# Kernel tuning notes

Measured on AMD Instinct MI355X. Metric: run time of the kernel, lower is better.

The kernel has to match this reference:

```python
import jax, jax.numpy as jnp
import numpy as np
import math

N_ENTITIES = 200000
N_ITEMS = 100000
N_REL = 40
DIM = 64
N_HEADS = 2
DK = DIM // N_HEADS
N_EDGES = 1500000
K_EDGES = 256
K_ITEMS = 100


def setup_inputs() -> dict:
    key = jax.random.key(0)
    k1, k2, k3, k4, k5, k6 = jax.random.split(key, 6)
    entity_emb = jax.random.normal(k1, (N_ENTITIES, DIM), jnp.float32) * 0.1
    W_Q = jax.random.normal(k2, (DIM, DIM), jnp.float32) * (1.0 / math.sqrt(DIM))
    relation_emb = jax.random.normal(k3, (N_REL - 1, DIM), jnp.float32) * 0.1
    edge_index = jax.random.randint(k4, (2, N_EDGES), 0, N_ENTITIES, jnp.int32)
    # edge_type in [1, N_REL-1]: code indexes relation_emb[edge_type - 1]
    edge_type = jax.random.randint(k5, (N_EDGES,), 1, N_REL, jnp.int32)
    # uniform(0,1) driving the gumbel noise -log(-log(u)); clipped away from 0
    noise_u = jax.random.uniform(k6, (N_EDGES,), jnp.float32, 1e-9, 1.0)
    return {"entity_emb": entity_emb, "W_Q": W_Q, "relation_emb": relation_emb,
            "noise_u": noise_u, "edge_index": edge_index, "edge_type": edge_type}


def reference(entity_emb, W_Q, relation_emb, noise_u, edge_index, edge_type):
    head, tail = edge_index[0], edge_index[1]
    E = edge_index.shape[1]

    # --- norm_attn_computer (AttnHGCN): per-edge multi-head attention ---
    # project once on nodes, then gather (same math as (emb[head] @ W_Q))
    proj = entity_emb @ W_Q                               # [N, D]
    q = proj[head].reshape(E, N_HEADS, DK)                # [E, H, Dk]
    k = proj[tail].reshape(E, N_HEADS, DK)                # [E, H, Dk]
    rel = relation_emb[edge_type - 1].reshape(E, N_HEADS, DK)
    attn = jnp.sum(q * k * rel, axis=-1) / math.sqrt(DK)  # [E, H]
    edge_attn_logits = attn.mean(axis=-1)                 # [E]

    # scatter_softmax over head nodes, then multiply by head degree (norm)
    seg_max = jax.lax.stop_gradient(
        jax.ops.segment_max(edge_attn_logits, head, num_segments=N_ENTITIES))
    ex = jnp.exp(edge_attn_logits - seg_max[head])
    denom = jax.ops.segment_sum(ex, head, num_segments=N_ENTITIES)
    edge_attn_score = ex / denom[head]
    deg = jax.ops.segment_sum(jnp.ones_like(edge_attn_logits), head,
                              num_segments=N_ENTITIES)
    edge_attn_score = edge_attn_score * deg[head]         # [E]

    # --- attn logit sums per item (head + tail scatter_sum), topk 100 ---
    sum_by_node = (jax.ops.segment_sum(edge_attn_logits, head, num_segments=N_ENTITIES)
                   + jax.ops.segment_sum(edge_attn_logits, tail, num_segments=N_ENTITIES))
    top_items_v, top_attn_items = jax.lax.top_k(sum_by_node[:N_ITEMS], K_ITEMS)

    # --- gumbel-noise injection + edge topk 256 ---
    noisy_score = edge_attn_score + (-jnp.log(-jnp.log(noise_u)))
    topk_v, topk_attn_edge_id = jax.lax.top_k(noisy_score, K_EDGES)

    return (edge_attn_score, topk_v, topk_attn_edge_id, top_items_v, top_attn_items)
```

## Files before the change

### kernel.cpp

```cpp
#include <hip/hip_runtime.h>

#define N_ENTITIES 200000
#define N_ITEMS    100000
#define DIM        64
#define N_EDGES    1500000
#define K_EDGES    256
#define K_ITEMS    100
#define SCALE      0.08838834764831845f

#define CAND_CAP   8192
#define NSCANB     ((N_ENTITIES + 255) / 256)

typedef unsigned long long u64;


__device__ __forceinline__ unsigned fkey(float x) {
    unsigned u = __float_as_uint(x);
    return (u & 0x80000000u) ? ~u : (u | 0x80000000u);
}
__device__ __forceinline__ float funkey(unsigned k) {
    return (k & 0x80000000u) ? __uint_as_float(k & 0x7fffffffu)
                             : __uint_as_float(~k);
}

__device__ __forceinline__ void lds_hist_add(unsigned* h, unsigned bin, bool valid, int lane) {
    bool need = valid;
    for (;;) {
        unsigned long long mask = __ballot(need);
        if (mask == 0ull) break;
        int leader = __ffsll(mask) - 1;
        unsigned lbin = __shfl(bin, leader, 64);
        bool same = need && (bin == lbin);
        unsigned long long grp = __ballot(same);
        if (lane == leader) atomicAdd(&h[lbin], (unsigned)__popcll(grp));
        need = need && !same;
    }
}

__device__ __forceinline__ unsigned select_digit(const unsigned* __restrict__ hist,
                                                 unsigned Keff, unsigned* above) {
    unsigned cum = 0;
    int b = 255;
    for (; b > 0; --b) {
        unsigned hb = hist[b];
        if (cum + hb >= Keff) break;
        cum += hb;
    }
    *above = cum;
    return (unsigned)b;
}

__global__ __launch_bounds__(256) void proj_kernel(const float* __restrict__ emb,
                                                   const float* __restrict__ W,
                                                   float* __restrict__ proj,
                                                   const int* __restrict__ head,
                                                   unsigned* __restrict__ degi,
                                                   unsigned* __restrict__ rank) {
    int e = blockIdx.x * blockDim.x + threadIdx.x;
    unsigned rk = 0;
    bool haveEdge = (e < N_EDGES);
    if (haveEdge) rk = atomicAdd(&degi[head[e]], 1u);

    __shared__ float part[4][16][64];
    const int t = threadIdx.x;
    const int c = t & 63;
    const int q = __builtin_amdgcn_readfirstlane(t >> 6);

    float Wreg[16];
#pragma unroll
    for (int j = 0; j < 16; ++j) Wreg[j] = W[(q * 16 + j) * 64 + c];

    const int base = blockIdx.x * 16;
    const float* erow = emb + (size_t)base * 64 + q * 16;

    float acc[16];
#pragma unroll
    for (int r = 0; r < 16; ++r) acc[r] = 0.f;
#pragma unroll
    for (int r = 0; r < 16; ++r) {
#pragma unroll
        for (int j = 0; j < 16; ++j)
            acc[r] += erow[r * 64 + j] * Wreg[j];
    }
#pragma unroll
    for (int r = 0; r < 16; ++r) part[q][r][c] = acc[r];
    __syncthreads();
#pragma unroll
    for (int it = 0; it < 4; ++it) {
        int oi = t + it * 256;
        int r = oi >> 6, cc = oi & 63;
        float s = part[0][r][cc] + part[1][r][cc] + part[2][r][cc] + part[3][r][cc];
        proj[(size_t)(base + r) * 64 + cc] = s;
    }
    if (haveEdge) rank[e] = rk;
}

__global__ void scan1_kernel(const unsigned* __restrict__ degi, unsigned* __restrict__ start,
                             unsigned* __restrict__ bsum) {
    __shared__ unsigned s[256];
    int t = threadIdx.x, i = blockIdx.x * 256 + t;
    unsigned v = (i < N_ENTITIES) ? degi[i] : 0u;
    s[t] = v;
    __syncthreads();
    for (int off = 1; off < 256; off <<= 1) {
        unsigned x = s[t];
        unsigned y = (t >= off) ? s[t - off] : 0u;
        __syncthreads();
        s[t] = x + y;
        __syncthreads();
    }
    if (i < N_ENTITIES) start[i] = s[t] - v;
    if (t == 255) bsum[blockIdx.x] = s[t];
}

__global__ __launch_bounds__(256) void scan23_kernel(const unsigned* __restrict__ bsum,
                                                     unsigned* __restrict__ start) {
    __shared__ unsigned part[4];
    const int b = blockIdx.x;
    const int t = threadIdx.x;
    unsigned s = 0;
    for (int j = t; j < b; j += 256) s += bsum[j];
#pragma unroll
    for (int off = 1; off < 64; off <<= 1) s += __shfl_xor(s, off, 64);
    if ((t & 63) == 0) part[t >> 6] = s;
    __syncthreads();
    unsigned prefix = part[0] + part[1] + part[2] + part[3];
    int i = b * 256 + t;
    if (i < N_ENTITIES) start[i] += prefix;
}

__global__ void scatter_kernel(const int* __restrict__ head, const int* __restrict__ tail,
                               const int* __restrict__ etype,
                               unsigned* __restrict__ rank,
                               const unsigned* __restrict__ start,
                               u64* __restrict__ rec, int csrMode) {
    int i = blockIdx.x * blockDim.x + threadIdx.x;
    if (i >= N_EDGES) return;
    unsigned slot = start[head[i]] + rank[i];
    u64 R = ((u64)(unsigned)tail[i] << 27) | ((u64)(unsigned)(etype[i] - 1) << 21) | (u64)(unsigned)i;
    rec[slot] = R;
    if (csrMode) rank[i] = slot;
}

__global__ __launch_bounds__(256) void node_pass(const float4* __restrict__ proj4,
                                                 const float4* __restrict__ rel4,
                                                 const u64* __restrict__ rec,
                                                 const unsigned* __restrict__ start,
                                                 const unsigned* __restrict__ degi,
                                                 float* __restrict__ logitsOut,
                                                 int csrMode,
                                                 float2* __restrict__ nd,
                                                 float* __restrict__ sumhead,
                                                 float* __restrict__ sumtailR,
                                                 int repMask) {
    unsigned xcd;
    asm volatile("s_getreg_b32 %0, hwreg(HW_REG_XCC_ID)" : "=s"(xcd));
    float* st = sumtailR + (size_t)(xcd & (unsigned)repMask) * N_ITEMS;

    int wave = (blockIdx.x * blockDim.x + threadIdx.x) >> 6;
    int lane = threadIdx.x & 63;
    int slot = lane >> 4, sl = lane & 15;
    unsigned s = start[wave], len = degi[wave];
    float4 ph = proj4[(size_t)wave * 16 + sl];
    float dsum = 0.f, lsum = 0.f;
    for (unsigned k0 = 0; k0 < len; k0 += 8) {
        unsigned ka = k0 + slot, kb = ka + 4;
        bool va = (ka < len), vb = (kb < len);
        u64 Ra = rec[s + (va ? ka : 0u)];
        u64 Rb = rec[s + (vb ? kb : 0u)];
        unsigned ta = (unsigned)(Ra >> 27), ria = ((unsigned)(Ra >> 21)) & 63u;
        unsigned tb = (unsigned)(Rb >> 27), rib = ((unsigned)(Rb >> 21)) & 63u;
        unsigned ea = (unsigned)Ra & 0x1FFFFFu, eb = (unsigned)Rb & 0x1FFFFFu;
        float4 pa = proj4[(size_t)ta * 16 + sl];
        float4 qa = rel4[(size_t)ria * 16 + sl];
        float4 pb = proj4[(size_t)tb * 16 + sl];
        float4 qb = rel4[(size_t)rib * 16 + sl];
        float xa = ph.x * pa.x * qa.x + ph.y * pa.y * qa.y + ph.z * pa.z * qa.z + ph.w * pa.w * qa.w;
        float xb = ph.x * pb.x * qb.x + ph.y * pb.y * qb.y + ph.z * pb.z * qb.z + ph.w * pb.w * qb.w;
        xa += __shfl_xor(xa, 1, 64);  xb += __shfl_xor(xb, 1, 64);
        xa += __shfl_xor(xa, 2, 64);  xb += __shfl_xor(xb, 2, 64);
        xa += __shfl_xor(xa, 4, 64);  xb += __shfl_xor(xb, 4, 64);
        xa += __shfl_xor(xa, 8, 64);  xb += __shfl_xor(xb, 8, 64);
        if (sl == 0) {
            if (va) {
                float lg = xa * SCALE;
                logitsOut[csrMode ? (s + ka) : ea] = lg;
                dsum += __expf(lg);
                lsum += lg;
                if (ta < N_ITEMS) atomicAdd(&st[ta], lg);
            }
            if (vb) {
                float lg = xb * SCALE;
                logitsOut[csrMode ? (s + kb) : eb] = lg;
                dsum += __expf(lg);
                lsum += lg;
                if (tb < N_ITEMS) atomicAdd(&st[tb], lg);
            }
        }
    }
    dsum += __shfl_xor(dsum, 16, 64);
    dsum += __shfl_xor(dsum, 32, 64);
    lsum += __shfl_xor(lsum, 16, 64);
    lsum += __shfl_xor(lsum, 32, 64);
    if (lane == 0) {
        nd[wave] = make_float2(dsum, (float)len);
        sumhead[wave] = lsum;
    }
}

__global__ void edge_pass3(const float* __restrict__ logitsEdge,
                           const float* __restrict__ logitsCsr,
                           const unsigned* __restrict__ slotmap, int csrMode,
                           const int* __restrict__ head,
                           const float2* __restrict__ nd, const float* __restrict__ noise_u,
                           const float* __restrict__ sumhead, const float* __restrict__ sumtailR,
                           int R,
                           float* __restrict__ out_scores, unsigned* __restrict__ keysE,
                           unsigned* __restrict__ keysI, unsigned* __restrict__ hists) {
    __shared__ unsigned hE[256];
    __shared__ unsigned hI[256];
    for (int j = threadIdx.x; j < 256; j += blockDim.x) { hE[j] = 0; hI[j] = 0; }
    __syncthreads();
    int i = blockIdx.x * blockDim.x + threadIdx.x;
    int lane = threadIdx.x & 63;

    unsigned bin = 0;
    bool valid = (i < N_EDGES);
    if (valid) {
        float lg = csrMode ? logitsCsr[slotmap[i]] : logitsEdge[i];
        float2 dd = nd[head[i]];
        float score = __expf(lg) / dd.x * dd.y;
        out_scores[i] = score;
        float noise = -logf(-logf(noise_u[i]));
        unsigned k = fkey(score + noise);
        keysE[i] = k;
        bin = k >> 24;
    }
    lds_hist_add(hE, bin, valid, lane);

    bin = 0;
    valid = (i < N_ITEMS);
    if (valid) {
        float s = sumhead[i];
        for (int r = 0; r < R; ++r) s += sumtailR[(size_t)r * N_ITEMS + i];
        unsigned k = fkey(s);
        keysI[i] = k;
        bin = k >> 24;
    }
    lds_hist_add(hI, bin, valid, lane);

    __syncthreads();
    for (int j = threadIdx.x; j < 256; j += blockDim.x) {
        unsigned v = hE[j];
        if (v) atomicAdd(&hists[j], v);
        v = hI[j];
        if (v) atomicAdd(&hists[3 * 256 + j], v);
    }
}

__global__ void collect_kernel(const unsigned* __restrict__ keysE,
                               const unsigned* __restrict__ keysI,
                               const unsigned* __restrict__ hists,
                               unsigned* __restrict__ counters, unsigned* __restrict__ cand) {
    const int y = blockIdx.y;
    const unsigned* keys = y ? keysI : keysE;
    const int n = y ? N_ITEMS : N_EDGES;
    const unsigned K = y ? K_ITEMS : K_EDGES;
    const unsigned* H = hists + (size_t)y * 3 * 256;
    unsigned aboveA;
    unsigned binA = select_digit(H, K, &aboveA);
    const unsigned T = binA << 24;
    unsigned* cd = cand + (size_t)y * 2 * CAND_CAP;

    int i = blockIdx.x * blockDim.x + threadIdx.x;
    int stride = gridDim.x * blockDim.x;
    for (; i < n; i += stride) {
        unsigned k = keys[i];
        if (k >= T) {
            unsigned p = atomicAdd(&counters[y], 1u);
            if (p < (unsigned)CAND_CAP) { cd[2 * p] = k; cd[2 * p + 1] = (unsigned)i; }
        }
    }
}

__global__ void final_topk_kernel(const unsigned* __restrict__ cand,
                                  const unsigned* __restrict__ counters,
                                  float* __restrict__ out_topkv, float* __restrict__ out_topki,
                                  float* __restrict__ out_itemv, float* __restrict__ out_itemi) {
    __shared__ unsigned sk[CAND_CAP];
    __shared__ unsigned si[CAND_CAP];
    const int y = blockIdx.x;
    const int K = y ? K_ITEMS : K_EDGES;
    float* outv = y ? out_itemv : out_topkv;
    float* outi = y ? out_itemi : out_topki;
    const unsigned* cd = cand + (size_t)y * 2 * CAND_CAP;
    unsigned m = counters[y];
    if (m > (unsigned)CAND_CAP) m = CAND_CAP;
    for (unsigned i = threadIdx.x; i < m; i += blockDim.x) {
        sk[i] = cd[2 * i];
        si[i] = cd[2 * i + 1];
    }
    __syncthreads();
    for (unsigned i = threadIdx.x; i < m; i += blockDim.x) {
        unsigned ki = sk[i], xi = si[i];
        int r = 0;
        for (unsigned j = 0; j < m; ++j) {
            unsigned kj = sk[j];
            if (kj > ki || (kj == ki && si[j] < xi)) r++;
        }
        if (r < K) {
            outv[r] = funkey(ki);
            outi[r] = (float)xi;
        }
    }
}

extern "C" void kernel_launch(void* const* d_in, const int* in_sizes, int n_in,
                              void* d_out, int out_size, void* d_ws, size_t ws_size,
                              hipStream_t stream) {
    (void)in_sizes; (void)n_in; (void)out_size;
    const float* emb    = (const float*)d_in[0];
    const float* W      = (const float*)d_in[1];
    const float* rel    = (const float*)d_in[2];
    const float* noise  = (const float*)d_in[3];
    const int*   eidx   = (const int*)d_in[4];
    const int*   etype  = (const int*)d_in[5];
    const int* head = eidx;
    const int* tail = eidx + N_EDGES;

    float* out        = (float*)d_out;
    float* out_scores = out;
    float* out_topkv  = out + N_EDGES;
    float* out_topki  = out + N_EDGES + K_EDGES;
    float* out_itemv  = out + N_EDGES + 2 * K_EDGES;
    float* out_itemi  = out + N_EDGES + 2 * K_EDGES + K_ITEMS;

    auto layout_floats = [](int R, int csr) -> size_t {
        return (size_t)N_ENTITIES * DIM + N_EDGES + 2 * (size_t)N_EDGES
             + N_ENTITIES + N_ENTITIES + (size_t)R * N_ITEMS
             + 2 * 3 * 256 + 2 + 2 * (size_t)N_ENTITIES + N_ENTITIES
             + 1024 + 2 * 2 * CAND_CAP + (csr ? (size_t)N_EDGES : 0);
    };
    int R = 8, csr = 1;
    while (R > 1 && ws_size < layout_floats(R, 1) * 4) R >>= 1;
    if (ws_size < layout_floats(1, 1) * 4) {
        csr = 0;
        R = 8;
        while (R > 1 && ws_size < layout_floats(R, 0) * 4) R >>= 1;
    }

    float* ws = (float*)d_ws;
    size_t o = 0;
    float*    proj    = ws + o;               o += (size_t)N_ENTITIES * DIM;
    unsigned* rank    = (unsigned*)(ws + o);
    float*    logits  = ws + o;               o += N_EDGES;
    u64*      rec     = (u64*)(ws + o);       o += 2 * (size_t)N_EDGES;
    unsigned* keysE   = (unsigned*)rec;
    unsigned* keysI   = keysE + N_EDGES;
    unsigned* start   = (unsigned*)(ws + o);  o += N_ENTITIES;
    unsigned* degi    = (unsigned*)(ws + o);  o += N_ENTITIES;
    float*    sumtailR= ws + o;               o += (size_t)R * N_ITEMS;
    unsigned* hists   = (unsigned*)(ws + o);  o += 2 * 3 * 256;
    unsigned* counters= (unsigned*)(ws + o);  o += 2;
    float2*   nd      = (float2*)(ws + o);    o += 2 * (size_t)N_ENTITIES;
    float*    sumhead = ws + o;               o += N_ENTITIES;
    unsigned* bsum    = (unsigned*)(ws + o);  o += 1024;
    unsigned* cand    = (unsigned*)(ws + o);  o += 2 * 2 * CAND_CAP;
    float*    logitsCsr = ws + o;             if (csr) o += N_EDGES;

    float*    nodePassLogits = csr ? logitsCsr : logits;

    hipMemsetAsync(degi, 0,
                   ((size_t)N_ENTITIES + (size_t)R * N_ITEMS + 2 * 3 * 256 + 2) * 4, stream);
    hipLaunchKernelGGL(proj_kernel, dim3(12500), dim3(256), 0, stream,
                       emb, W, proj, head, degi, rank);
    hipLaunchKernelGGL(scan1_kernel, dim3(NSCANB), dim3(256), 0, stream, degi, start, bsum);
    hipLaunchKernelGGL(scan23_kernel, dim3(NSCANB), dim3(256), 0, stream, bsum, start);
    hipLaunchKernelGGL(scatter_kernel, dim3((N_EDGES + 255) / 256), dim3(256), 0, stream,
                       head, tail, etype, rank, start, rec, csr);
    hipLaunchKernelGGL(node_pass, dim3(N_ENTITIES / 4), dim3(256), 0, stream,
                       (const float4*)proj, (const float4*)rel, rec, start, degi,
                       nodePassLogits, csr, nd, sumhead, sumtailR, R - 1);
    hipLaunchKernelGGL(edge_pass3, dim3((N_EDGES + 255) / 256), dim3(256), 0, stream,
                       logits, logitsCsr, rank, csr, head, (const float2*)nd, noise,
                       sumhead, sumtailR, R,
                       out_scores, keysE, keysI, hists);
    hipLaunchKernelGGL(collect_kernel, dim3(512, 2), dim3(256), 0, stream,
                       keysE, keysI, hists, counters, cand);
    hipLaunchKernelGGL(final_topk_kernel, dim3(2), dim3(1024), 0, stream,
                       cand, counters, out_topkv, out_topki, out_itemv, out_itemi);
}
```

Measured before the change: 504.7 us.

## Privatize per-node degree counters per XCD to cut cross-die atomic contention

The degree-count atomics in proj_kernel now go to eight per-XCD counter arrays, and the XCD id is packed into the high bits of each edge's rank. The scan kernels merge these per-XCD counts into total degrees and compute per-XCD start offsets, which scatter_kernel uses to place each CSR record. The aim is to keep atomics local to each die's L2 and avoid coherence traffic across dies. In exchange the memset is 8x larger, the scans touch 8x more counter memory, and the workspace grows by 7*N_ENTITIES words.

```diff
diff --git a/kernel.cpp b/kernel.cpp
--- a/kernel.cpp
+++ b/kernel.cpp
@@ -10,6 +10,7 @@
 
 #define CAND_CAP   8192
 #define NSCANB     ((N_ENTITIES + 255) / 256)
+#define NXCD       8
 
 typedef unsigned long long u64;
 
@@ -54,12 +55,16 @@
                                                    const float* __restrict__ W,
                                                    float* __restrict__ proj,
                                                    const int* __restrict__ head,
-                                                   unsigned* __restrict__ degi,
+                                                   unsigned* __restrict__ degiX,
                                                    unsigned* __restrict__ rank) {
+    unsigned xcd;
+    asm volatile("s_getreg_b32 %0, hwreg(HW_REG_XCC_ID)" : "=s"(xcd));
+    xcd &= (NXCD - 1);
+
     int e = blockIdx.x * blockDim.x + threadIdx.x;
     unsigned rk = 0;
     bool haveEdge = (e < N_EDGES);
-    if (haveEdge) rk = atomicAdd(&degi[head[e]], 1u);
+    if (haveEdge) rk = (xcd << 28) | atomicAdd(&degiX[(size_t)xcd * N_ENTITIES + head[e]], 1u);
 
     __shared__ float part[4][16][64];
     const int t = threadIdx.x;
@@ -95,12 +100,26 @@
     if (haveEdge) rank[e] = rk;
 }
 
-__global__ void scan1_kernel(const unsigned* __restrict__ degi, unsigned* __restrict__ start,
+__global__ void scan1_kernel(unsigned* __restrict__ degiX,
+                             unsigned* __restrict__ degtot,
+                             unsigned* __restrict__ start,
                              unsigned* __restrict__ bsum) {
     __shared__ unsigned s[256];
     int t = threadIdx.x, i = blockIdx.x * 256 + t;
-    unsigned v = (i < N_ENTITIES) ? degi[i] : 0u;
-    s[t] = v;
+    unsigned tot = 0;
+    if (i < N_ENTITIES) {
+        unsigned px[NXCD];
+#pragma unroll
+        for (int x = 0; x < NXCD; ++x) {
+            px[x] = tot;
+            tot += degiX[(size_t)x * N_ENTITIES + i];
+        }
+#pragma unroll
+        for (int x = 0; x < NXCD; ++x)
+            degiX[(size_t)x * N_ENTITIES + i] = px[x];
+        degtot[i] = tot;
+    }
+    s[t] = tot;
     __syncthreads();
     for (int off = 1; off < 256; off <<= 1) {
         unsigned x = s[t];
@@ -109,12 +128,13 @@
         s[t] = x + y;
         __syncthreads();
     }
-    if (i < N_ENTITIES) start[i] = s[t] - v;
+    if (i < N_ENTITIES) start[i] = s[t] - tot;
     if (t == 255) bsum[blockIdx.x] = s[t];
 }
 
 __global__ __launch_bounds__(256) void scan23_kernel(const unsigned* __restrict__ bsum,
-                                                     unsigned* __restrict__ start) {
+                                                     unsigned* __restrict__ start,
+                                                     unsigned* __restrict__ degiX) {
     __shared__ unsigned part[4];
     const int b = blockIdx.x;
     const int t = threadIdx.x;
@@ -126,17 +146,25 @@
     __syncthreads();
     unsigned prefix = part[0] + part[1] + part[2] + part[3];
     int i = b * 256 + t;
-    if (i < N_ENTITIES) start[i] += prefix;
+    if (i < N_ENTITIES) {
+        unsigned sg = start[i] + prefix;
+        start[i] = sg;
+#pragma unroll
+        for (int x = 0; x < NXCD; ++x)
+            degiX[(size_t)x * N_ENTITIES + i] += sg;
+    }
 }
 
 __global__ void scatter_kernel(const int* __restrict__ head, const int* __restrict__ tail,
                                const int* __restrict__ etype,
                                unsigned* __restrict__ rank,
-                               const unsigned* __restrict__ start,
+                               const unsigned* __restrict__ startX,
                                u64* __restrict__ rec, int csrMode) {
     int i = blockIdx.x * blockDim.x + threadIdx.x;
     if (i >= N_EDGES) return;
-    unsigned slot = start[head[i]] + rank[i];
+    unsigned r = rank[i];
+    unsigned x = r >> 28;
+    unsigned slot = startX[(size_t)x * N_ENTITIES + head[i]] + (r & 0x0FFFFFFFu);
     u64 R = ((u64)(unsigned)tail[i] << 27) | ((u64)(unsigned)(etype[i] - 1) << 21) | (u64)(unsigned)i;
     rec[slot] = R;
     if (csrMode) rank[i] = slot;
@@ -146,7 +174,7 @@
                                                  const float4* __restrict__ rel4,
                                                  const u64* __restrict__ rec,
                                                  const unsigned* __restrict__ start,
-                                                 const unsigned* __restrict__ degi,
+                                                 const unsigned* __restrict__ degtot,
                                                  float* __restrict__ logitsOut,
                                                  int csrMode,
                                                  float2* __restrict__ nd,
@@ -160,7 +188,7 @@
     int wave = (blockIdx.x * blockDim.x + threadIdx.x) >> 6;
     int lane = threadIdx.x & 63;
     int slot = lane >> 4, sl = lane & 15;
-    unsigned s = start[wave], len = degi[wave];
+    unsigned s = start[wave], len = degtot[wave];
     float4 ph = proj4[(size_t)wave * 16 + sl];
     float dsum = 0.f, lsum = 0.f;
     for (unsigned k0 = 0; k0 < len; k0 += 8) {
@@ -337,7 +365,8 @@
 
     auto layout_floats = [](int R, int csr) -> size_t {
         return (size_t)N_ENTITIES * DIM + N_EDGES + 2 * (size_t)N_EDGES
-             + N_ENTITIES + N_ENTITIES + (size_t)R * N_ITEMS
+             + N_ENTITIES + (size_t)NXCD * N_ENTITIES + N_ENTITIES
+             + (size_t)R * N_ITEMS
              + 2 * 3 * 256 + 2 + 2 * (size_t)N_ENTITIES + N_ENTITIES
              + 1024 + 2 * 2 * CAND_CAP + (csr ? (size_t)N_EDGES : 0);
     };
@@ -358,7 +387,8 @@
     unsigned* keysE   = (unsigned*)rec;
     unsigned* keysI   = keysE + N_EDGES;
     unsigned* start   = (unsigned*)(ws + o);  o += N_ENTITIES;
-    unsigned* degi    = (unsigned*)(ws + o);  o += N_ENTITIES;
+    unsigned* degtot  = (unsigned*)(ws + o);  o += N_ENTITIES;
+    unsigned* degiX   = (unsigned*)(ws + o);  o += (size_t)NXCD * N_ENTITIES;
     float*    sumtailR= ws + o;               o += (size_t)R * N_ITEMS;
     unsigned* hists   = (unsigned*)(ws + o);  o += 2 * 3 * 256;
     unsigned* counters= (unsigned*)(ws + o);  o += 2;
@@ -370,16 +400,19 @@
 
     float*    nodePassLogits = csr ? logitsCsr : logits;
 
-    hipMemsetAsync(degi, 0,
-                   ((size_t)N_ENTITIES + (size_t)R * N_ITEMS + 2 * 3 * 256 + 2) * 4, stream);
+    hipMemsetAsync(degiX, 0,
+                   ((size_t)NXCD * N_ENTITIES + (size_t)R * N_ITEMS + 2 * 3 * 256 + 2) * 4,
+                   stream);
     hipLaunchKernelGGL(proj_kernel, dim3(12500), dim3(256), 0, stream,
-                       emb, W, proj, head, degi, rank);
-    hipLaunchKernelGGL(scan1_kernel, dim3(NSCANB), dim3(256), 0, stream, degi, start, bsum);
-    hipLaunchKernelGGL(scan23_kernel, dim3(NSCANB), dim3(256), 0, stream, bsum, start);
+                       emb, W, proj, head, degiX, rank);
+    hipLaunchKernelGGL(scan1_kernel, dim3(NSCANB), dim3(256), 0, stream,
+                       degiX, degtot, start, bsum);
+    hipLaunchKernelGGL(scan23_kernel, dim3(NSCANB), dim3(256), 0, stream,
+                       bsum, start, degiX);
     hipLaunchKernelGGL(scatter_kernel, dim3((N_EDGES + 255) / 256), dim3(256), 0, stream,
-                       head, tail, etype, rank, start, rec, csr);
+                       head, tail, etype, rank, degiX, rec, csr);
     hipLaunchKernelGGL(node_pass, dim3(N_ENTITIES / 4), dim3(256), 0, stream,
-                       (const float4*)proj, (const float4*)rel, rec, start, degi,
+                       (const float4*)proj, (const float4*)rel, rec, start, degtot,
                        nodePassLogits, csr, nd, sumhead, sumtailR, R - 1);
     hipLaunchKernelGGL(edge_pass3, dim3((N_EDGES + 255) / 256), dim3(256), 0, stream,
                        logits, logitsCsr, rank, csr, head, (const float2*)nd, noise,
```

New measurement: 514.8 us. About the same (+2.0%).
